# Kernel tuning notes

Measured on AMD Instinct MI355X. Metric: run time of the kernel, lower is better.

The kernel has to match this reference:

```python
import jax, jax.numpy as jnp
import numpy as np

B, T_OUT, S_IN, D, H, L = 256, 36, 96, 1024, 1024, 2  # batch, out_seq_len, in_seq_len, out_dim, hidden_dim, num_layer


def setup_inputs() -> dict:
    key = jax.random.key(0)
    ks = jax.random.split(key, 12)
    s = 0.02  # param init scale
    return {
        "target": jax.random.normal(ks[0], (B, T_OUT, D), jnp.float32),
        "hidden": jax.random.normal(ks[1], (L, B, H), jnp.float32),
        "enc_output": jax.random.normal(ks[2], (B, S_IN, H), jnp.float32),
        # attn_weight: Linear(D+H -> S_IN)
        "attn_w_W": jax.random.normal(ks[3], (S_IN, D + H), jnp.float32) * s,
        "attn_w_b": jnp.zeros((S_IN,), jnp.float32),
        # attn_combine: Linear(D+H -> D)
        "comb_W": jax.random.normal(ks[4], (D, D + H), jnp.float32) * s,
        "comb_b": jnp.zeros((D,), jnp.float32),
        # GRU weights stacked over layers (valid since D == H)
        "W_ih": jax.random.normal(ks[5], (L, 3 * H, D), jnp.float32) * s,
        "W_hh": jax.random.normal(ks[6], (L, 3 * H, H), jnp.float32) * s,
        "b_ih": jnp.zeros((L, 3 * H), jnp.float32),
        "b_hh": jnp.zeros((L, 3 * H), jnp.float32),
        # out: Linear(H -> D) then Linear(D -> D)
        "out1_W": jax.random.normal(ks[7], (D, H), jnp.float32) * s,
        "out1_b": jnp.zeros((D,), jnp.float32),
        "out2_W": jax.random.normal(ks[8], (D, D), jnp.float32) * s,
        "out2_b": jnp.zeros((D,), jnp.float32),
    }


def _gru_cell(x, h, Wi, Wh, bi, bh):
    # PyTorch GRU cell: r,z,n gate ordering
    gi = x @ Wi.T + bi  # (B, 3H)
    gh = h @ Wh.T + bh  # (B, 3H)
    i_r, i_z, i_n = jnp.split(gi, 3, axis=-1)
    h_r, h_z, h_n = jnp.split(gh, 3, axis=-1)
    r = jax.nn.sigmoid(i_r + h_r)
    z = jax.nn.sigmoid(i_z + h_z)
    n = jnp.tanh(i_n + r * h_n)
    return (1.0 - z) * n + z * h


def reference(target, hidden, enc_output, attn_w_W, attn_w_b, comb_W, comb_b,
              W_ih, W_hh, b_ih, b_hh, out1_W, out1_b, out2_W, out2_b):
    # Teacher-forcing branch (teacher_forcing_ratio = 1.0): input at step i is target[:, i, :]
    n_layers = hidden.shape[0]

    def step(h_carry, x):
        # x: (B, D); h_carry: (L, B, H)
        cat1 = jnp.concatenate([x, h_carry[-1]], axis=-1)           # (B, D+H)
        aw = jax.nn.softmax(cat1 @ attn_w_W.T + attn_w_b, axis=-1)  # (B, S_IN)
        w_enc = jnp.einsum('bs,bsh->bh', aw, enc_output)            # (B, H)
        xc = jax.nn.relu(jnp.concatenate([x, w_enc], -1) @ comb_W.T + comb_b)  # (B, D)
        hs = []
        inp = xc
        for l in range(n_layers):  # small fixed layer count
            hl = _gru_cell(inp, h_carry[l], W_ih[l], W_hh[l], b_ih[l], b_hh[l])
            hs.append(hl)
            inp = hl
        new_h = jnp.stack(hs, axis=0)
        y = (inp @ out1_W.T + out1_b) @ out2_W.T + out2_b           # (B, D)
        return new_h, (y, aw)

    hidden_f, (ys, aws) = jax.lax.scan(step, hidden, jnp.swapaxes(target, 0, 1))
    output = jnp.swapaxes(ys, 0, 1)        # (B, T_OUT, D)
    attn_weights = jnp.swapaxes(aws, 0, 1)  # (B, T_OUT, S_IN)
    return output, hidden_f, attn_weights
```

## Files before the change

kernel.cpp:

```cpp
#include <hip/hip_runtime.h>
#include <hip/hip_bf16.h>
#include <stdint.h>

typedef unsigned short u16;
typedef unsigned int   u32;
typedef unsigned long long ull;
typedef __attribute__((ext_vector_type(8))) short short8;
typedef __attribute__((ext_vector_type(4))) float f32x4;
typedef __attribute__((ext_vector_type(16))) float f32x16;

#define T_OUT 36
#define NB    256
#define S_IN  96
#define DD    1024
#define HH    1024

#define OFF_HID  9437184
#define OFF_ATTN 9961472

enum { EPI_BF16 = 2, EPI_YOUT = 3, EPI_YBATCH = 4, EPI_SCX = 5, EPI_CX = 6,
       EPI_COMB2 = 7 };

__device__ __forceinline__ float b2f(u16 u) {
    return __uint_as_float(((u32)u) << 16);
}
__device__ __forceinline__ u16 f2b(float f) {
    __hip_bfloat16 h = __float2bfloat16(f);
    return __builtin_bit_cast(unsigned short, h);
}

template <int RAW>
__device__ __forceinline__ short8 ld8(const void* p, size_t eoff, bool isbf) {
    if (RAW == 0 || isbf) {
        return *(const short8*)((const u16*)p + eoff);
    } else {
        const float* f = (const float*)p + eoff;
        short8 r;
        #pragma unroll
        for (int i = 0; i < 8; ++i) r[i] = (short)f2b(f[i]);
        return r;
    }
}

__global__ __launch_bounds__(256) void k_detect(const u32* __restrict__ t,
                                                int* __restrict__ flag)
{
    __shared__ int cnt[256];
    u32 w = t[threadIdx.x];
    int e = (w >> 7) & 0xFF;
    cnt[threadIdx.x] = (e >= 100 && e <= 140) ? 1 : 0;
    __syncthreads();
    for (int s = 128; s > 0; s >>= 1) {
        if (threadIdx.x < s) cnt[threadIdx.x] += cnt[threadIdx.x + s];
        __syncthreads();
    }
    if (threadIdx.x == 0) flag[0] = (cnt[0] >= 128) ? 1 : 0;
}

__global__ __launch_bounds__(256) void k_cvt16(const void* __restrict__ src,
                                               u16* __restrict__ dst, int n4,
                                               const int* __restrict__ flagp)
{
    const int i = blockIdx.x * 256 + threadIdx.x;
    if (i >= n4) return;
    if (*flagp) {
        ((ull*)dst)[i] = ((const ull*)src)[i];
    } else {
        f32x4 v = ((const f32x4*)src)[i];
        ull pk = (ull)f2b(v[0]) | ((ull)f2b(v[1]) << 16)
               | ((ull)f2b(v[2]) << 32) | ((ull)f2b(v[3]) << 48);
        ((ull*)dst)[i] = pk;
    }
}

__global__ __launch_bounds__(256) void k_cvtf(const void* __restrict__ src,
                                              float* __restrict__ dst, int n,
                                              const int* __restrict__ flagp)
{
    const int i = blockIdx.x * 256 + threadIdx.x;
    if (i >= n) return;
    dst[i] = *flagp ? b2f(((const u16*)src)[i]) : ((const float*)src)[i];
}

__global__ __launch_bounds__(256) void k_trcvt(const void* __restrict__ in,
                                               u16* __restrict__ out,
                                               int ldin, int col0,
                                               const int* __restrict__ flagp)
{
    const bool isbf = (*flagp != 0);
    __shared__ u16 tile[64][65];
    const int bx = blockIdx.x * 64, by = blockIdx.y * 64;
    const int c = threadIdx.x & 63, r0 = threadIdx.x >> 6;
    #pragma unroll
    for (int rr = 0; rr < 16; ++rr) {
        int r = r0 * 16 + rr;
        size_t idx = (size_t)(by + r) * ldin + col0 + bx + c;
        tile[r][c] = isbf ? ((const u16*)in)[idx] : f2b(((const float*)in)[idx]);
    }
    __syncthreads();
    #pragma unroll
    for (int rr = 0; rr < 16; ++rr) {
        int r = r0 * 16 + rr;
        out[(size_t)(bx + r) * 1024 + by + c] = tile[c][r];
    }
}

__global__ __launch_bounds__(256) void k_bc(const void* __restrict__ W2,
                                            const void* __restrict__ b1,
                                            const void* __restrict__ b2,
                                            float* __restrict__ bc,
                                            const int* __restrict__ flagp)
{
    const bool isbf = (*flagp != 0);
    const int lane = threadIdx.x & 63;
    const int d = blockIdx.x * 4 + (threadIdx.x >> 6);
    float s = 0.f;
    if (isbf) {
        const u16* wr = (const u16*)W2 + (size_t)d * 1024 + lane * 16;
        const u16* bb = (const u16*)b1 + lane * 16;
        #pragma unroll
        for (int c = 0; c < 2; ++c) {
            short8 a = *(const short8*)(wr + c * 8);
            short8 v = *(const short8*)(bb + c * 8);
            #pragma unroll
            for (int e = 0; e < 8; ++e) s += b2f((u16)a[e]) * b2f((u16)v[e]);
        }
    } else {
        const float* wr = (const float*)W2 + (size_t)d * 1024 + lane * 16;
        const float* bb = (const float*)b1 + lane * 16;
        #pragma unroll
        for (int c = 0; c < 4; ++c) {
            f32x4 a = *(const f32x4*)(wr + c * 4);
            f32x4 v = *(const f32x4*)(bb + c * 4);
            s += a[0]*v[0] + a[1]*v[1] + a[2]*v[2] + a[3]*v[3];
        }
    }
    #pragma unroll
    for (int dd = 32; dd > 0; dd >>= 1) s += __shfl_xor(s, dd, 64);
    if (lane == 0) {
        float b2v = isbf ? b2f(((const u16*)b2)[d]) : ((const float*)b2)[d];
        bc[d] = s + b2v;
    }
}

template <int EPI, int RAWA, int RAWB>
__global__ __launch_bounds__(128) void k_gemm(
    const void* __restrict__ A, const void* __restrict__ B, void* __restrict__ Cp,
    int lda, int ldb, int M, int N, int K,
    const float* __restrict__ fbias, int t, int ldc,
    const int* __restrict__ flagp, size_t boff, const void* __restrict__ Xadd)
{
    const bool isbf = (*flagp != 0);
    __shared__ short8 As[64 * 4];
    __shared__ short8 Bs[128 * 4];

    const int tid  = threadIdx.x;
    const int lane = tid & 63;
    const int w    = tid >> 6;
    const int bm   = blockIdx.x * 64;
    const int bn   = blockIdx.y * 128;

    const int srow = tid >> 2;
    const int sg   = tid & 3;
    const int m0   = lane & 31;
    const int kq   = lane >> 5;

    f32x16 acc[2][2];
    #pragma unroll
    for (int i = 0; i < 2; ++i)
        #pragma unroll
        for (int j = 0; j < 2; ++j) acc[i][j] = (f32x16)0.0f;

    short8 av[2], bv[4];
    auto LOADG = [&](int kt) {
        const int k0 = kt << 5;
        #pragma unroll
        for (int i = 0; i < 2; ++i) {
            int r = srow + 32 * i;
            av[i] = ld8<RAWA>(A, (size_t)(bm + r) * lda + k0 + sg * 8, isbf);
        }
        #pragma unroll
        for (int i = 0; i < 4; ++i) {
            int gr = bn + srow + 32 * i;
            if (gr < N) bv[i] = ld8<RAWB>(B, boff + (size_t)gr * ldb + k0 + sg * 8, isbf);
            else        bv[i] = (short8)(short)0;
        }
    };

    const int kiter = K >> 5;
    LOADG(0);
    for (int kt = 0; kt < kiter; ++kt) {
        __syncthreads();
        #pragma unroll
        for (int i = 0; i < 2; ++i) {
            int r = srow + 32 * i;
            As[r * 4 + (sg ^ (r & 3))] = av[i];
        }
        #pragma unroll
        for (int i = 0; i < 4; ++i) {
            int r = srow + 32 * i;
            Bs[r * 4 + (sg ^ (r & 3))] = bv[i];
        }
        __syncthreads();
        if (kt + 1 < kiter) LOADG(kt + 1);
        #pragma unroll
        for (int ks = 0; ks < 2; ++ks) {
            const int gk = ks * 2 + kq;
            short8 af[2], bf[2];
            #pragma unroll
            for (int i = 0; i < 2; ++i) {
                int r = i * 32 + m0;
                af[i] = As[r * 4 + (gk ^ (r & 3))];
            }
            #pragma unroll
            for (int j = 0; j < 2; ++j) {
                int r = w * 64 + j * 32 + m0;
                bf[j] = Bs[r * 4 + (gk ^ (r & 3))];
            }
            #pragma unroll
            for (int i = 0; i < 2; ++i)
                #pragma unroll
                for (int j = 0; j < 2; ++j)
                    acc[i][j] = __builtin_amdgcn_mfma_f32_32x32x16_bf16(
                        af[i], bf[j], acc[i][j], 0, 0, 0);
        }
    }

    #pragma unroll
    for (int i = 0; i < 2; ++i) {
        #pragma unroll
        for (int j = 0; j < 2; ++j) {
            #pragma unroll
            for (int reg = 0; reg < 16; ++reg) {
                int row = (reg & 3) + 8 * (reg >> 2) + 4 * kq;
                int gr = bm + i * 32 + row;
                int gc = bn + w * 64 + j * 32 + m0;
                if (gc < N) {
                    float v = acc[i][j][reg];
                    if constexpr (EPI == EPI_COMB2) {
                        size_t cidx = ((size_t)gr * T_OUT + t) * DD + gc;
                        float cx = isbf ? b2f(((const u16*)Xadd)[cidx])
                                        : ((const float*)Xadd)[cidx];
                        v += fbias[gc] + cx;
                        v = fmaxf(v, 0.0f);
                        ((u16*)Cp)[(size_t)gr * ldc + gc] = f2b(v);
                    } else if constexpr (EPI == EPI_BF16) {
                        ((u16*)Cp)[(size_t)gr * ldc + gc] = f2b(v);
                    } else if constexpr (EPI == EPI_SCX) {
                        size_t oidx = (size_t)OFF_ATTN + (size_t)gr * ldc + gc;
                        if (isbf) ((u16*)Cp)[oidx] = f2b(v);
                        else      ((float*)Cp)[oidx] = v;
                    } else if constexpr (EPI == EPI_CX) {
                        if (isbf) ((u16*)Cp)[(size_t)gr * ldc + gc] = f2b(v);
                        else      ((float*)Cp)[(size_t)gr * ldc + gc] = v;
                    } else if constexpr (EPI == EPI_YOUT) {
                        v += fbias[gc];
                        size_t oidx = (size_t)gr * (T_OUT * DD) + (size_t)t * DD + gc;
                        if (isbf) ((u16*)Cp)[oidx] = f2b(v);
                        else      ((float*)Cp)[oidx] = v;
                    } else {
                        v += fbias[gc];
                        int tt = gr >> 8, bb = gr & 255;
                        size_t oidx = (size_t)bb * (T_OUT * DD) + (size_t)tt * DD + gc;
                        if (isbf) ((u16*)Cp)[oidx] = f2b(v);
                        else      ((float*)Cp)[oidx] = v;
                    }
                }
            }
        }
    }
}

template <int RAWB>
__global__ __launch_bounds__(256) void k_gruf(
    const u16* __restrict__ X, const u16* __restrict__ Hin,
    const void* __restrict__ Wih, const void* __restrict__ Whh, size_t w_eoff,
    const float* __restrict__ biF, const float* __restrict__ bhF,
    float* __restrict__ hfl, u16* __restrict__ Hout,
    u16* __restrict__ hist, int t, const int* __restrict__ flagp)
{
    const bool isbf = (*flagp != 0);
    __shared__ __align__(16) char smem[49152];

    const int tid  = threadIdx.x;
    const int g    = tid >> 7;
    const int tid2 = tid & 127;
    short8* Xs = (short8*)(smem + g * 20480);
    short8* Hs = (short8*)(smem + g * 20480 + 4096);
    short8* Ws = (short8*)(smem + g * 20480 + 8192);
    float*  Pp = (float*)smem;

    const int lane = tid2 & 63;
    const int w    = tid2 >> 6;
    const int J0   = blockIdx.x * 32;
    const int bm   = blockIdx.y * 64;
    const int m0   = lane & 31;
    const int kq   = lane >> 5;

    f32x16 acc[6];
    #pragma unroll
    for (int q = 0; q < 6; ++q) acc[q] = (f32x16)0.0f;

    const int srr = tid2 >> 2;
    const int sg  = tid2 & 3;

    short8 xv[2], hv[2], wv[6];
    auto LOAD = [&](int kt) {
        const int k0 = kt << 5;
        #pragma unroll
        for (int i = 0; i < 2; ++i) {
            int idx = i * 128 + tid2;
            int row = idx >> 2, gg = idx & 3;
            xv[i] = *(const short8*)(X   + (size_t)(bm + row) * 1024 + k0 + gg * 8);
            hv[i] = *(const short8*)(Hin + (size_t)(bm + row) * 1024 + k0 + gg * 8);
        }
        #pragma unroll
        for (int i = 0; i < 6; ++i) {
            int gate = (i < 3) ? i : i - 3;
            const void* mat = (i < 3) ? Wih : Whh;
            size_t grow = (size_t)(gate * 1024 + J0 + srr);
            wv[i] = ld8<RAWB>(mat, w_eoff + grow * 1024 + k0 + sg * 8, isbf);
        }
    };

    const int kt0 = g * 16;
    LOAD(kt0);
    for (int i = 0; i < 16; ++i) {
        __syncthreads();
        #pragma unroll
        for (int ii = 0; ii < 2; ++ii) {
            int idx = ii * 128 + tid2;
            int row = idx >> 2, gg = idx & 3;
            Xs[row * 4 + (gg ^ (row & 3))] = xv[ii];
            Hs[row * 4 + (gg ^ (row & 3))] = hv[ii];
        }
        #pragma unroll
        for (int ii = 0; ii < 6; ++ii) {
            Ws[(ii * 32 + srr) * 4 + (sg ^ (srr & 3))] = wv[ii];
        }
        __syncthreads();
        if (i < 15) LOAD(kt0 + i + 1);
        #pragma unroll
        for (int ks = 0; ks < 2; ++ks) {
            const int gk = ks * 2 + kq;
            const int r = w * 32 + m0;
            short8 ax = Xs[r * 4 + (gk ^ (r & 3))];
            short8 ah = Hs[r * 4 + (gk ^ (r & 3))];
            short8 bw[6];
            #pragma unroll
            for (int q = 0; q < 6; ++q)
                bw[q] = Ws[(q * 32 + m0) * 4 + (gk ^ (m0 & 3))];
            acc[0] = __builtin_amdgcn_mfma_f32_32x32x16_bf16(ax, bw[0], acc[0], 0, 0, 0);
            acc[1] = __builtin_amdgcn_mfma_f32_32x32x16_bf16(ax, bw[1], acc[1], 0, 0, 0);
            acc[2] = __builtin_amdgcn_mfma_f32_32x32x16_bf16(ax, bw[2], acc[2], 0, 0, 0);
            acc[3] = __builtin_amdgcn_mfma_f32_32x32x16_bf16(ah, bw[3], acc[3], 0, 0, 0);
            acc[4] = __builtin_amdgcn_mfma_f32_32x32x16_bf16(ah, bw[4], acc[4], 0, 0, 0);
            acc[5] = __builtin_amdgcn_mfma_f32_32x32x16_bf16(ah, bw[5], acc[5], 0, 0, 0);
        }
    }

    __syncthreads();
    if (g == 1) {
        #pragma unroll
        for (int q = 0; q < 6; ++q)
            #pragma unroll
            for (int reg = 0; reg < 16; ++reg)
                Pp[(q * 16 + reg) * 128 + tid2] = acc[q][reg];
    }
    __syncthreads();
    if (g == 0) {
        #pragma unroll
        for (int q = 0; q < 6; ++q)
            #pragma unroll
            for (int reg = 0; reg < 16; ++reg)
                acc[q][reg] += Pp[(q * 16 + reg) * 128 + tid2];

        const int jg = J0 + m0;
        const float bir = biF[jg],         bhr = bhF[jg];
        const float biz = biF[1024 + jg],  bhz = bhF[1024 + jg];
        const float bin_ = biF[2048 + jg], bhn = bhF[2048 + jg];
        #pragma unroll
        for (int reg = 0; reg < 16; ++reg) {
            int row = (reg & 3) + 8 * (reg >> 2) + 4 * kq;
            int bb = bm + w * 32 + row;
            float ir  = acc[0][reg] + bir;
            float iz  = acc[1][reg] + biz;
            float in_ = acc[2][reg] + bin_;
            float hr  = acc[3][reg] + bhr;
            float hz  = acc[4][reg] + bhz;
            float hn  = acc[5][reg] + bhn;
            float r = 1.f / (1.f + expf(-(ir + hr)));
            float z = 1.f / (1.f + expf(-(iz + hz)));
            float n = tanhf(in_ + r * hn);
            size_t hidx = (size_t)bb * 1024 + jg;
            float hold = hfl ? hfl[hidx] : b2f(Hin[hidx]);
            float hnew = (1.f - z) * n + z * hold;
            if (hfl) hfl[hidx] = hnew;
            u16 h16 = f2b(hnew);
            Hout[hidx] = h16;
            if (hist) hist[(size_t)(t * NB + bb) * HH + jg] = h16;
        }
    }
}

__global__ __launch_bounds__(1024) void k_attn(
    const u16* __restrict__ hb1, const u16* __restrict__ attnWB,
    const float* __restrict__ attnBF, const void* __restrict__ enc,
    const u16* __restrict__ encW, const u16* __restrict__ W2t,
    const float* __restrict__ combBF, u16* __restrict__ xc,
    u16* __restrict__ wencG, void* __restrict__ d_out,
    const int* __restrict__ flagp, int t)
{
    const bool isbf = (*flagp != 0);
    __shared__ float sc[S_IN];
    __shared__ float pst[8][1024];
    __shared__ float wencS[1024];
    const int tid  = threadIdx.x;
    const int b    = blockIdx.x;
    const int w    = tid >> 6;
    const int lane = tid & 63;

    short8 h0v = *(const short8*)(hb1 + (size_t)b * HH + lane * 8);
    short8 h1v = *(const short8*)(hb1 + (size_t)b * HH + 512 + lane * 8);
    float hr[16];
    #pragma unroll
    for (int e = 0; e < 8; ++e) {
        hr[e]     = b2f((u16)h0v[e]);
        hr[8 + e] = b2f((u16)h1v[e]);
    }

    #pragma unroll
    for (int i = 0; i < 6; ++i) {
        const int s = w * 6 + i;
        const u16* wr = attnWB + (size_t)s * 2048 + 1024 + (size_t)lane * 8;
        float p = 0.f;
        #pragma unroll
        for (int c = 0; c < 2; ++c) {
            short8 v = *(const short8*)(wr + c * 512);
            #pragma unroll
            for (int e = 0; e < 8; ++e) p += hr[c * 8 + e] * b2f((u16)v[e]);
        }
        #pragma unroll
        for (int d = 32; d > 0; d >>= 1) p += __shfl_xor(p, d, 64);
        if (lane == 0) {
            size_t sidx = (size_t)OFF_ATTN + ((size_t)b * T_OUT + t) * S_IN + s;
            float sx = isbf ? b2f(((const u16*)d_out)[sidx])
                            : ((const float*)d_out)[sidx];
            sc[s] = p + attnBF[s] + sx;
        }
    }
    __syncthreads();

    if (w == 0) {
        float a  = sc[lane];
        float bq = (lane < 32) ? sc[64 + lane] : -3.0e38f;
        float m = fmaxf(a, bq);
        #pragma unroll
        for (int d = 32; d > 0; d >>= 1) m = fmaxf(m, __shfl_xor(m, d, 64));
        float e0 = expf(a - m);
        float e1 = (lane < 32) ? expf(bq - m) : 0.f;
        float ss = e0 + e1;
        #pragma unroll
        for (int d = 32; d > 0; d >>= 1) ss += __shfl_xor(ss, d, 64);
        float inv = 1.f / ss;
        sc[lane] = e0 * inv;
        if (lane < 32) sc[64 + lane] = e1 * inv;
    }
    __syncthreads();

    if (tid < S_IN) {
        float a = sc[tid];
        size_t aidx = (size_t)OFF_ATTN + ((size_t)b * T_OUT + t) * S_IN + tid;
        if (isbf) ((u16*)d_out)[aidx] = f2b(a);
        else      ((float*)d_out)[aidx] = a;
    }

    const int rg = tid >> 7;
    const int hx = (tid & 127) * 8;

    if (encW) {
        float acc[8] = {0.f, 0.f, 0.f, 0.f, 0.f, 0.f, 0.f, 0.f};
        const u16* eb = encW + (size_t)b * S_IN * HH + hx;
        #pragma unroll
        for (int it = 0; it < 12; ++it) {
            const int s = it * 8 + rg;
            const float aw = sc[s];
            short8 v = *(const short8*)(eb + (size_t)s * HH);
            #pragma unroll
            for (int e = 0; e < 8; ++e) acc[e] += aw * b2f((u16)v[e]);
        }
        #pragma unroll
        for (int e = 0; e < 8; ++e) pst[rg][hx + e] = acc[e];
        __syncthreads();
        float s = pst[0][tid];
        #pragma unroll
        for (int r2 = 1; r2 < 8; ++r2) s += pst[r2][tid];
        size_t cidx = ((size_t)b * T_OUT + t) * DD + tid;
        float cx = isbf ? b2f(((const u16*)d_out)[cidx])
                        : ((const float*)d_out)[cidx];
        float v = fmaxf(cx + combBF[tid] + s, 0.f);
        xc[(size_t)b * DD + tid] = f2b(v);
        return;
    }

    float acc[8] = {0.f, 0.f, 0.f, 0.f, 0.f, 0.f, 0.f, 0.f};
    if (isbf) {
        const u16* eb = (const u16*)enc + (size_t)b * S_IN * HH + hx;
        #pragma unroll
        for (int it = 0; it < 12; ++it) {
            const int s = it * 8 + rg;
            const float aw = sc[s];
            short8 v = *(const short8*)(eb + (size_t)s * HH);
            #pragma unroll
            for (int e = 0; e < 8; ++e) acc[e] += aw * b2f((u16)v[e]);
        }
    } else {
        const float* eb = (const float*)enc + (size_t)b * S_IN * HH + hx;
        #pragma unroll
        for (int it = 0; it < 12; ++it) {
            const int s = it * 8 + rg;
            const float aw = sc[s];
            f32x4 v0 = *(const f32x4*)(eb + (size_t)s * HH);
            f32x4 v1 = *(const f32x4*)(eb + (size_t)s * HH + 4);
            acc[0] += aw * v0[0]; acc[1] += aw * v0[1];
            acc[2] += aw * v0[2]; acc[3] += aw * v0[3];
            acc[4] += aw * v1[0]; acc[5] += aw * v1[1];
            acc[6] += aw * v1[2]; acc[7] += aw * v1[3];
        }
    }
    #pragma unroll
    for (int e = 0; e < 8; ++e) pst[rg][hx + e] = acc[e];
    __syncthreads();
    {
        float s = pst[0][tid];
        #pragma unroll
        for (int r2 = 1; r2 < 8; ++r2) s += pst[r2][tid];
        wencS[tid] = s;
    }
    __syncthreads();

    if (W2t) {
        const int dq = tid & 255;
        const int kg = tid >> 8;
        const int d4 = dq * 4;
        float a0 = 0.f, a1 = 0.f, a2 = 0.f, a3 = 0.f;
        const u16* wp = W2t + (size_t)(kg * 256) * 1024 + d4;
        const float* ws = wencS + kg * 256;
        #pragma unroll 8
        for (int k = 0; k < 256; ++k) {
            float wv = ws[k];
            ull m = *(const ull*)(wp + (size_t)k * 1024);
            a0 += wv * b2f((u16)(m));
            a1 += wv * b2f((u16)(m >> 16));
            a2 += wv * b2f((u16)(m >> 32));
            a3 += wv * b2f((u16)(m >> 48));
        }
        float* P2 = &pst[0][0];
        P2[kg * 1024 + d4 + 0] = a0;
        P2[kg * 1024 + d4 + 1] = a1;
        P2[kg * 1024 + d4 + 2] = a2;
        P2[kg * 1024 + d4 + 3] = a3;
        __syncthreads();
        float s2 = P2[tid] + P2[1024 + tid] + P2[2048 + tid] + P2[3072 + tid];
        size_t cidx = ((size_t)b * T_OUT + t) * DD + tid;
        float cx = isbf ? b2f(((const u16*)d_out)[cidx])
                        : ((const float*)d_out)[cidx];
        float v = fmaxf(cx + combBF[tid] + s2, 0.f);
        xc[(size_t)b * DD + tid] = f2b(v);
    } else {
        wencG[(size_t)b * HH + tid] = f2b(wencS[tid]);
    }
}

__global__ __launch_bounds__(256) void k_init(const void* __restrict__ hid,
                                              float* __restrict__ hf,
                                              u16* __restrict__ hb,
                                              const int* __restrict__ flagp)
{
    const int i = blockIdx.x * 256 + threadIdx.x;
    float v = *flagp ? b2f(((const u16*)hid)[i]) : ((const float*)hid)[i];
    if (hf) hf[i] = v;
    hb[i] = f2b(v);
}

__global__ __launch_bounds__(256) void k_hidout(const float* __restrict__ hf,
                                                const u16* __restrict__ hb,
                                                void* __restrict__ d_out,
                                                const int* __restrict__ flagp)
{
    const int i = blockIdx.x * 256 + threadIdx.x;
    float v = hf ? hf[i] : b2f(hb[i]);
    if (*flagp) ((u16*)d_out)[OFF_HID + i] = f2b(v);
    else        ((float*)d_out)[OFF_HID + i] = v;
}

extern "C" void kernel_launch(void* const* d_in, const int* in_sizes, int n_in,
                              void* d_out, int out_size, void* d_ws, size_t ws_size,
                              hipStream_t stream)
{
    const void* target = d_in[0];
    const void* hidden = d_in[1];
    const void* enc    = d_in[2];
    const void* attnW  = d_in[3];
    const void* attnB  = d_in[4];
    const void* combW  = d_in[5];
    const void* combB  = d_in[6];
    const void* Wih    = d_in[7];
    const void* Whh    = d_in[8];
    const void* bih    = d_in[9];
    const void* bhh    = d_in[10];
    const void* out1W  = d_in[11];
    const void* out1B  = d_in[12];
    const void* out2W  = d_in[13];
    const void* out2B  = d_in[14];

    char* ws = (char*)d_ws;
    size_t off = 0;
    #define WSALLOC(name, type, bytes) type* name = (type*)(ws + off); off += (((size_t)(bytes)) + 255) & ~(size_t)255;
    WSALLOC(flag,   int,   256)
    WSALLOC(xcat,   u16,   256*2048*2)
    WSALLOC(xc,     u16,   256*1024*2)
    WSALLOC(hbq,    u16,   2*2*256*1024*2)
    WSALLOC(Wc,     u16,   1024*1024*2)
    WSALLOC(attnWB, u16,   96*2048*2)
    WSALLOC(attnBF, float, 128*4)
    WSALLOC(combBF, float, 1024*4)
    WSALLOC(bihF,   float, 2*3072*4)
    WSALLOC(bhhF,   float, 2*3072*4)
    WSALLOC(bc,     float, 1024*4)
    WSALLOC(W1t,    u16,   1024*1024*2)
    size_t off_nohf = off;
    WSALLOC(hf,     float, 2*256*1024*4)
    size_t off_core = off;
    WSALLOC(WihB,   u16,   2*3072*1024*2)
    WSALLOC(WhhB,   u16,   2*3072*1024*2)
    WSALLOC(combW2t,u16,   1024*2048*2)
    size_t off_big = off;
    WSALLOC(Hist,   u16,   36*256*1024*2)
    size_t off_hist = off;
    WSALLOC(encW,   u16,   256*96*1024*2)
    size_t off_encw = off;
    #undef WSALLOC
    (void)off_nohf;

    const bool useHf   = (ws_size >= off_core);
    const bool BIG     = (ws_size >= off_big);
    const bool useHist = (ws_size >= off_hist);
    const bool useEncW = (ws_size >= off_encw);
    if (!useHf) hf = nullptr;

    int hostbf = -1;
    if (in_sizes) {
        long long tb = (long long)in_sizes[0];
        const long long n_t = (long long)NB * T_OUT * DD;
        if (tb == n_t * 2) hostbf = 1;
        else if (tb == n_t * 4) hostbf = 0;
    }
    const bool RAWOK = (hostbf == 1);

    k_detect<<<1, 256, 0, stream>>>((const u32*)target, flag);
    k_init<<<2048, 256, 0, stream>>>(hidden, hf, hbq, flag);

    const u16* attnWx = (const u16*)attnW;
    if (!RAWOK) {
        k_cvt16<<<192, 256, 0, stream>>>(attnW, attnWB, 96*2048/4, flag);
        attnWx = attnWB;
    }
    k_cvtf<<<1, 256, 0, stream>>>(attnB, attnBF, 96, flag);
    k_cvtf<<<4, 256, 0, stream>>>(combB, combBF, 1024, flag);
    k_cvtf<<<24, 256, 0, stream>>>(bih, bihF, 6144, flag);
    k_cvtf<<<24, 256, 0, stream>>>(bhh, bhhF, 6144, flag);
    k_trcvt<<<dim3(16, 16), 256, 0, stream>>>(out1W, W1t, 1024, 0, flag);
    if (BIG && !useEncW) {
        k_trcvt<<<dim3(16, 16), 256, 0, stream>>>(combW, combW2t, 2048, 1024, flag);
    }

    if (RAWOK) {
        k_gemm<EPI_BF16, 0, 0><<<dim3(16, 8, 1), 128, 0, stream>>>(
            out2W, W1t, Wc, 1024, 1024, 1024, 1024, 1024, nullptr, 0, 1024,
            flag, 0, nullptr);
    } else if (BIG) {
        u16* out2Wb = WihB;
        k_cvt16<<<1024, 256, 0, stream>>>(out2W, out2Wb, 1024*1024/4, flag);
        k_gemm<EPI_BF16, 0, 0><<<dim3(16, 8, 1), 128, 0, stream>>>(
            out2Wb, W1t, Wc, 1024, 1024, 1024, 1024, 1024, nullptr, 0, 1024,
            flag, 0, nullptr);
    } else {
        k_gemm<EPI_BF16, 1, 0><<<dim3(16, 8, 1), 128, 0, stream>>>(
            out2W, W1t, Wc, 1024, 1024, 1024, 1024, 1024, nullptr, 0, 1024,
            flag, 0, nullptr);
    }
    k_bc<<<256, 256, 0, stream>>>(out2W, out1B, out2B, bc, flag);

    const void* WihP = Wih;
    const void* WhhP = Whh;
    bool gru_u16 = RAWOK;
    if (!RAWOK && BIG) {
        k_cvt16<<<6144, 256, 0, stream>>>(Wih, WihB, 2*3072*1024/4, flag);
        k_cvt16<<<6144, 256, 0, stream>>>(Whh, WhhB, 2*3072*1024/4, flag);
        WihP = WihB; WhhP = WhhB; gru_u16 = true;
    }

    k_gemm<EPI_CX, 1, 1><<<dim3(144, 8, 1), 128, 0, stream>>>(
        target, combW, d_out, 1024, 2048, 9216, 1024, 1024, nullptr, 0, 1024,
        flag, 0, nullptr);
    k_gemm<EPI_SCX, 1, 1><<<dim3(144, 1, 1), 128, 0, stream>>>(
        target, attnW, d_out, 1024, 2048, 9216, 96, 1024, nullptr, 0, 96,
        flag, 0, nullptr);
    if (useEncW) {
        k_gemm<EPI_BF16, 1, 1><<<dim3(384, 8, 1), 128, 0, stream>>>(
            enc, combW, encW, 1024, 2048, 24576, 1024, 1024, nullptr, 0, 1024,
            flag, 1024, nullptr);
    }

    const size_t L1 = 3072ull * 1024ull;
    const int BUF = 2 * 256 * 1024;
    for (int t = 0; t < T_OUT; ++t) {
        u16* bi = hbq + (t & 1) * BUF;
        u16* bo = hbq + ((t + 1) & 1) * BUF;
        k_attn<<<256, 1024, 0, stream>>>(bi + 262144, attnWx, attnBF, enc,
                                         useEncW ? encW : nullptr,
                                         (BIG && !useEncW) ? combW2t : nullptr,
                                         combBF, xc, xcat, d_out, flag, t);
        if (!BIG && !useEncW) {
            k_gemm<EPI_COMB2, 0, 1><<<dim3(4, 8, 1), 128, 0, stream>>>(
                xcat, combW, xc, 1024, 2048, 256, 1024, 1024, combBF, t, 1024,
                flag, 1024, d_out);
        }
        if (gru_u16) {
            k_gruf<0><<<dim3(32, 4), 256, 0, stream>>>(
                xc, bi, WihP, WhhP, 0, bihF, bhhF, hf, bo, nullptr, t, flag);
            k_gruf<0><<<dim3(32, 4), 256, 0, stream>>>(
                bo, bi + 262144, WihP, WhhP, L1, bihF + 3072, bhhF + 3072,
                hf ? hf + 262144 : nullptr, bo + 262144,
                useHist ? Hist : nullptr, t, flag);
        } else {
            k_gruf<1><<<dim3(32, 4), 256, 0, stream>>>(
                xc, bi, Wih, Whh, 0, bihF, bhhF, hf, bo, nullptr, t, flag);
            k_gruf<1><<<dim3(32, 4), 256, 0, stream>>>(
                bo, bi + 262144, Wih, Whh, L1, bihF + 3072, bhhF + 3072,
                hf ? hf + 262144 : nullptr, bo + 262144,
                useHist ? Hist : nullptr, t, flag);
        }
        if (!useHist) {
            k_gemm<EPI_YOUT, 0, 0><<<dim3(4, 8, 1), 128, 0, stream>>>(
                bo + 262144, Wc, d_out, 1024, 1024, 256, 1024, 1024, bc, t, 1024,
                flag, 0, nullptr);
        }
    }

    if (useHist) {
        k_gemm<EPI_YBATCH, 0, 0><<<dim3(144, 8, 1), 128, 0, stream>>>(
            Hist, Wc, d_out, 1024, 1024, 9216, 1024, 1024, bc, 0, 1024,
            flag, 0, nullptr);
    }
    k_hidout<<<2048, 256, 0, stream>>>(hf, hbq, d_out, flag);
}
```

Measured before the change: 3.155 ms.

## Enlarge GEMM tiles to 128x128 and split GRU K-loop across four warp groups

The generic GEMM kernel moves from a 64x128 tile with 2 waves to a 128x128 tile with 4 waves arranged 2x2, with padded LDS rows (stride 5) and launch grids halved to match. The fused GRU kernel doubles its threads to 512, splitting the K reduction into four groups of 8 iterations instead of two of 16. Partial sums are then reduced through LDS in two passes. This aims to improve operand reuse and latency hiding in the per-step recurrent GEMMs. In exchange it adds LDS use (80KB), extra reduction syncs, and fewer blocks for the small per-step GEMMs.

```diff
diff --git a/kernel.cpp b/kernel.cpp
--- a/kernel.cpp
+++ b/kernel.cpp
@@ -144,20 +144,21 @@
 }
 
 template <int EPI, int RAWA, int RAWB>
-__global__ __launch_bounds__(128) void k_gemm(
+__global__ __launch_bounds__(256) void k_gemm(
     const void* __restrict__ A, const void* __restrict__ B, void* __restrict__ Cp,
     int lda, int ldb, int M, int N, int K,
     const float* __restrict__ fbias, int t, int ldc,
     const int* __restrict__ flagp, size_t boff, const void* __restrict__ Xadd)
 {
     const bool isbf = (*flagp != 0);
-    __shared__ short8 As[64 * 4];
-    __shared__ short8 Bs[128 * 4];
+    __shared__ short8 As[128 * 5];
+    __shared__ short8 Bs[128 * 5];
 
     const int tid  = threadIdx.x;
     const int lane = tid & 63;
     const int w    = tid >> 6;
-    const int bm   = blockIdx.x * 64;
+    const int wr   = w >> 1, wc = w & 1;
+    const int bm   = blockIdx.x * 128;
     const int bn   = blockIdx.y * 128;
 
     const int srow = tid >> 2;
@@ -171,17 +172,14 @@
         #pragma unroll
         for (int j = 0; j < 2; ++j) acc[i][j] = (f32x16)0.0f;
 
-    short8 av[2], bv[4];
+    short8 av[2], bv[2];
     auto LOADG = [&](int kt) {
         const int k0 = kt << 5;
         #pragma unroll
         for (int i = 0; i < 2; ++i) {
-            int r = srow + 32 * i;
+            int r = srow + 64 * i;
             av[i] = ld8<RAWA>(A, (size_t)(bm + r) * lda + k0 + sg * 8, isbf);
-        }
-        #pragma unroll
-        for (int i = 0; i < 4; ++i) {
-            int gr = bn + srow + 32 * i;
+            int gr = bn + r;
             if (gr < N) bv[i] = ld8<RAWB>(B, boff + (size_t)gr * ldb + k0 + sg * 8, isbf);
             else        bv[i] = (short8)(short)0;
         }
@@ -193,13 +191,9 @@
         __syncthreads();
         #pragma unroll
         for (int i = 0; i < 2; ++i) {
-            int r = srow + 32 * i;
-            As[r * 4 + (sg ^ (r & 3))] = av[i];
-        }
-        #pragma unroll
-        for (int i = 0; i < 4; ++i) {
-            int r = srow + 32 * i;
-            Bs[r * 4 + (sg ^ (r & 3))] = bv[i];
+            int r = srow + 64 * i;
+            As[r * 5 + (sg ^ (r & 3))] = av[i];
+            Bs[r * 5 + (sg ^ (r & 3))] = bv[i];
         }
         __syncthreads();
         if (kt + 1 < kiter) LOADG(kt + 1);
@@ -209,13 +203,13 @@
             short8 af[2], bf[2];
             #pragma unroll
             for (int i = 0; i < 2; ++i) {
-                int r = i * 32 + m0;
-                af[i] = As[r * 4 + (gk ^ (r & 3))];
+                int r = wr * 64 + i * 32 + m0;
+                af[i] = As[r * 5 + (gk ^ (r & 3))];
             }
             #pragma unroll
             for (int j = 0; j < 2; ++j) {
-                int r = w * 64 + j * 32 + m0;
-                bf[j] = Bs[r * 4 + (gk ^ (r & 3))];
+                int r = wc * 64 + j * 32 + m0;
+                bf[j] = Bs[r * 5 + (gk ^ (r & 3))];
             }
             #pragma unroll
             for (int i = 0; i < 2; ++i)
@@ -233,8 +227,8 @@
             #pragma unroll
             for (int reg = 0; reg < 16; ++reg) {
                 int row = (reg & 3) + 8 * (reg >> 2) + 4 * kq;
-                int gr = bm + i * 32 + row;
-                int gc = bn + w * 64 + j * 32 + m0;
+                int gr = bm + wr * 64 + i * 32 + row;
+                int gc = bn + wc * 64 + j * 32 + m0;
                 if (gc < N) {
                     float v = acc[i][j][reg];
                     if constexpr (EPI == EPI_COMB2) {
@@ -272,7 +266,7 @@
 }
 
 template <int RAWB>
-__global__ __launch_bounds__(256) void k_gruf(
+__global__ __launch_bounds__(512) void k_gruf(
     const u16* __restrict__ X, const u16* __restrict__ Hin,
     const void* __restrict__ Wih, const void* __restrict__ Whh, size_t w_eoff,
     const float* __restrict__ biF, const float* __restrict__ bhF,
@@ -280,7 +274,7 @@
     u16* __restrict__ hist, int t, const int* __restrict__ flagp)
 {
     const bool isbf = (*flagp != 0);
-    __shared__ __align__(16) char smem[49152];
+    __shared__ __align__(16) char smem[81920];
 
     const int tid  = threadIdx.x;
     const int g    = tid >> 7;
@@ -323,9 +317,9 @@
         }
     };
 
-    const int kt0 = g * 16;
+    const int kt0 = g * 8;
     LOAD(kt0);
-    for (int i = 0; i < 16; ++i) {
+    for (int i = 0; i < 8; ++i) {
         __syncthreads();
         #pragma unroll
         for (int ii = 0; ii < 2; ++ii) {
@@ -339,7 +333,7 @@
             Ws[(ii * 32 + srr) * 4 + (sg ^ (srr & 3))] = wv[ii];
         }
         __syncthreads();
-        if (i < 15) LOAD(kt0 + i + 1);
+        if (i < 7) LOAD(kt0 + i + 1);
         #pragma unroll
         for (int ks = 0; ks < 2; ++ks) {
             const int gk = ks * 2 + kq;
@@ -360,20 +354,40 @@
     }
 
     __syncthreads();
-    if (g == 1) {
-        #pragma unroll
-        for (int q = 0; q < 6; ++q)
+    if (g != 0) {
+        #pragma unroll
+        for (int q = 0; q < 3; ++q)
             #pragma unroll
             for (int reg = 0; reg < 16; ++reg)
-                Pp[(q * 16 + reg) * 128 + tid2] = acc[q][reg];
+                Pp[((g - 1) * 3 + q) * 2048 + reg * 128 + tid2] = acc[q][reg];
     }
     __syncthreads();
     if (g == 0) {
         #pragma unroll
-        for (int q = 0; q < 6; ++q)
+        for (int q = 0; q < 3; ++q)
             #pragma unroll
             for (int reg = 0; reg < 16; ++reg)
-                acc[q][reg] += Pp[(q * 16 + reg) * 128 + tid2];
+                acc[q][reg] += Pp[(0 + q) * 2048 + reg * 128 + tid2]
+                             + Pp[(3 + q) * 2048 + reg * 128 + tid2]
+                             + Pp[(6 + q) * 2048 + reg * 128 + tid2];
+    }
+    __syncthreads();
+    if (g != 0) {
+        #pragma unroll
+        for (int q = 0; q < 3; ++q)
+            #pragma unroll
+            for (int reg = 0; reg < 16; ++reg)
+                Pp[((g - 1) * 3 + q) * 2048 + reg * 128 + tid2] = acc[3 + q][reg];
+    }
+    __syncthreads();
+    if (g == 0) {
+        #pragma unroll
+        for (int q = 0; q < 3; ++q)
+            #pragma unroll
+            for (int reg = 0; reg < 16; ++reg)
+                acc[3 + q][reg] += Pp[(0 + q) * 2048 + reg * 128 + tid2]
+                                 + Pp[(3 + q) * 2048 + reg * 128 + tid2]
+                                 + Pp[(6 + q) * 2048 + reg * 128 + tid2];
 
         const int jg = J0 + m0;
         const float bir = biF[jg],         bhr = bhF[jg];
@@ -676,17 +690,17 @@
     }
 
     if (RAWOK) {
-        k_gemm<EPI_BF16, 0, 0><<<dim3(16, 8, 1), 128, 0, stream>>>(
+        k_gemm<EPI_BF16, 0, 0><<<dim3(8, 8, 1), 256, 0, stream>>>(
             out2W, W1t, Wc, 1024, 1024, 1024, 1024, 1024, nullptr, 0, 1024,
             flag, 0, nullptr);
     } else if (BIG) {
         u16* out2Wb = WihB;
         k_cvt16<<<1024, 256, 0, stream>>>(out2W, out2Wb, 1024*1024/4, flag);
-        k_gemm<EPI_BF16, 0, 0><<<dim3(16, 8, 1), 128, 0, stream>>>(
+        k_gemm<EPI_BF16, 0, 0><<<dim3(8, 8, 1), 256, 0, stream>>>(
             out2Wb, W1t, Wc, 1024, 1024, 1024, 1024, 1024, nullptr, 0, 1024,
             flag, 0, nullptr);
     } else {
-        k_gemm<EPI_BF16, 1, 0><<<dim3(16, 8, 1), 128, 0, stream>>>(
+        k_gemm<EPI_BF16, 1, 0><<<dim3(8, 8, 1), 256, 0, stream>>>(
             out2W, W1t, Wc, 1024, 1024, 1024, 1024, 1024, nullptr, 0, 1024,
             flag, 0, nullptr);
     }
@@ -701,14 +715,14 @@
         WihP = WihB; WhhP = WhhB; gru_u16 = true;
     }
 
-    k_gemm<EPI_CX, 1, 1><<<dim3(144, 8, 1), 128, 0, stream>>>(
+    k_gemm<EPI_CX, 1, 1><<<dim3(72, 8, 1), 256, 0, stream>>>(
         target, combW, d_out, 1024, 2048, 9216, 1024, 1024, nullptr, 0, 1024,
         flag, 0, nullptr);
-    k_gemm<EPI_SCX, 1, 1><<<dim3(144, 1, 1), 128, 0, stream>>>(
+    k_gemm<EPI_SCX, 1, 1><<<dim3(72, 1, 1), 256, 0, stream>>>(
         target, attnW, d_out, 1024, 2048, 9216, 96, 1024, nullptr, 0, 96,
         flag, 0, nullptr);
     if (useEncW) {
-        k_gemm<EPI_BF16, 1, 1><<<dim3(384, 8, 1), 128, 0, stream>>>(
+        k_gemm<EPI_BF16, 1, 1><<<dim3(192, 8, 1), 256, 0, stream>>>(
             enc, combW, encW, 1024, 2048, 24576, 1024, 1024, nullptr, 0, 1024,
             flag, 1024, nullptr);
     }
@@ -723,34 +737,34 @@
                                          (BIG && !useEncW) ? combW2t : nullptr,
                                          combBF, xc, xcat, d_out, flag, t);
         if (!BIG && !useEncW) {
-            k_gemm<EPI_COMB2, 0, 1><<<dim3(4, 8, 1), 128, 0, stream>>>(
+            k_gemm<EPI_COMB2, 0, 1><<<dim3(2, 8, 1), 256, 0, stream>>>(
                 xcat, combW, xc, 1024, 2048, 256, 1024, 1024, combBF, t, 1024,
                 flag, 1024, d_out);
         }
         if (gru_u16) {
-            k_gruf<0><<<dim3(32, 4), 256, 0, stream>>>(
+            k_gruf<0><<<dim3(32, 4), 512, 0, stream>>>(
                 xc, bi, WihP, WhhP, 0, bihF, bhhF, hf, bo, nullptr, t, flag);
-            k_gruf<0><<<dim3(32, 4), 256, 0, stream>>>(
+            k_gruf<0><<<dim3(32, 4), 512, 0, stream>>>(
                 bo, bi + 262144, WihP, WhhP, L1, bihF + 3072, bhhF + 3072,
                 hf ? hf + 262144 : nullptr, bo + 262144,
                 useHist ? Hist : nullptr, t, flag);
         } else {
-            k_gruf<1><<<dim3(32, 4), 256, 0, stream>>>(
+            k_gruf<1><<<dim3(32, 4), 512, 0, stream>>>(
                 xc, bi, Wih, Whh, 0, bihF, bhhF, hf, bo, nullptr, t, flag);
-            k_gruf<1><<<dim3(32, 4), 256, 0, stream>>>(
+            k_gruf<1><<<dim3(32, 4), 512, 0, stream>>>(
                 bo, bi + 262144, Wih, Whh, L1, bihF + 3072, bhhF + 3072,
                 hf ? hf + 262144 : nullptr, bo + 262144,
                 useHist ? Hist : nullptr, t, flag);
         }
         if (!useHist) {
-            k_gemm<EPI_YOUT, 0, 0><<<dim3(4, 8, 1), 128, 0, stream>>>(
+            k_gemm<EPI_YOUT, 0, 0><<<dim3(2, 8, 1), 256, 0, stream>>>(
                 bo + 262144, Wc, d_out, 1024, 1024, 256, 1024, 1024, bc, t, 1024,
                 flag, 0, nullptr);
         }
     }
 
     if (useHist) {
-        k_gemm<EPI_YBATCH, 0, 0><<<dim3(144, 8, 1), 128, 0, stream>>>(
+        k_gemm<EPI_YBATCH, 0, 0><<<dim3(72, 8, 1), 256, 0, stream>>>(
             Hist, Wc, d_out, 1024, 1024, 9216, 1024, 1024, bc, 0, 1024,
             flag, 0, nullptr);
     }
```

New measurement: 3.210 ms. No clear change (+1.7%).
